# Performance work log

Measured on AMD Instinct MI355X. Metric: run time of the kernel, lower is better.

The kernel has to match this reference:

```python
import jax, jax.numpy as jnp
import numpy as np
from jax import lax

EPS = 1e-5

@jax.custom_vjp
def bin_active(x):
    # forward: sign binarization (original also returns channel-mean of |x|, which is discarded)
    return jnp.sign(x)

def _ba_fwd(x):
    return jnp.sign(x), x

def _ba_bwd(x, g):
    # straight-through estimator: zero grad where |x| >= 1
    return (jnp.where((x >= 1.0) | (x <= -1.0), 0.0, g),)

bin_active.defvjp(_ba_fwd, _ba_bwd)


def setup_inputs() -> dict:
    key = jax.random.key(0)
    k1, k2 = jax.random.split(key)
    N, C_in, H, W_sp = 64, 256, 56, 56
    C_out, K = 256, 3
    x = jax.random.normal(k1, (N, C_in, H, W_sp), dtype=jnp.float32)
    gamma = jnp.ones((C_in,), dtype=jnp.float32)
    beta = jnp.zeros((C_in,), dtype=jnp.float32)
    W = jax.random.normal(k2, (C_out, C_in, K, K), dtype=jnp.float32) * 0.05
    return {"x": x, "gamma": gamma, "beta": beta, "W": W}


def reference(x, gamma, beta, W):
    # BatchNorm2d (training-mode batch stats), affine
    mean = jnp.mean(x, axis=(0, 2, 3), keepdims=True)          # [1,C,1,1]
    var = jnp.var(x, axis=(0, 2, 3), keepdims=True)
    xn = (x - mean) * lax.rsqrt(var + EPS)
    xn = xn * gamma.reshape(1, -1, 1, 1) + beta.reshape(1, -1, 1, 1)
    # binarize activations
    xb = bin_active(xn)
    # Conv2d stride=1 pad=1, no bias, then ReLU
    y = lax.conv_general_dilated(
        xb, W,
        window_strides=(1, 1),
        padding=[(1, 1), (1, 1)],
        dimension_numbers=("NCHW", "OIHW", "NCHW"),
    )
    return jax.nn.relu(y)
```

## Files before the change

kernel.cpp:

```cpp
#include <hip/hip_runtime.h>
#include <hip/hip_bf16.h>
#include <stdint.h>

#define HP 58
#define WP 64
#define CIN 256
#define COUT 256
#define HH 56
#define WW 56
#define IMG_STRIDE (HP*WP*CIN)
#define ROW_STRIDE (WP*CIN)
#define NPIX 200704.0

#define XO    2048
#define XROW  14848
#define AO    93184
#define LDS_TOTAL 158720

typedef __attribute__((ext_vector_type(4))) int i32x4;

#define GLDS(g, l) __builtin_amdgcn_global_load_lds( \
    (const __attribute__((address_space(1))) void*)(g), \
    (__attribute__((address_space(3))) void*)(l), 16, 0, 0)

__global__ __launch_bounds__(256) void stats_partial(const float* __restrict__ x,
                                                     double* __restrict__ part) {
  int b = blockIdx.x;
  int c = b >> 6, n = b & 63;
  const float4* p = (const float4*)(x + (size_t)(n*CIN + c) * (HH*WW));
  double s = 0.0, s2 = 0.0;
  for (int i = threadIdx.x; i < 784; i += 256) {
    float4 v = p[i];
    double a0 = v.x, a1 = v.y, a2 = v.z, a3 = v.w;
    s  += (a0 + a1) + (a2 + a3);
    s2 += (a0*a0 + a1*a1) + (a2*a2 + a3*a3);
  }
  for (int off = 32; off > 0; off >>= 1) {
    s  += __shfl_down(s, off);
    s2 += __shfl_down(s2, off);
  }
  __shared__ double red[8];
  int wv = threadIdx.x >> 6, ln = threadIdx.x & 63;
  if (ln == 0) { red[wv*2] = s; red[wv*2+1] = s2; }
  __syncthreads();
  if (threadIdx.x == 0) {
    double ts = ((red[0]+red[2])+red[4])+red[6];
    double t2 = ((red[1]+red[3])+red[5])+red[7];
    part[(size_t)(c*64 + n)*2]     = ts;
    part[(size_t)(c*64 + n)*2 + 1] = t2;
  }
}

__global__ void stats_final(const double* __restrict__ part,
                            const float* __restrict__ gamma,
                            const float* __restrict__ beta,
                            double* __restrict__ prm) {
  int c = threadIdx.x;
  double s = 0.0, s2 = 0.0;
  for (int n = 0; n < 64; ++n) {
    s  += part[(size_t)(c*64+n)*2];
    s2 += part[(size_t)(c*64+n)*2 + 1];
  }
  double mean = s / NPIX;
  double var  = s2 / NPIX - mean*mean;
  double inv  = 1.0 / sqrt(var + 1e-5);
  prm[c*4+0] = mean;
  prm[c*4+1] = (double)gamma[c] * inv;
  prm[c*4+2] = (double)beta[c];
}

__global__ __launch_bounds__(256) void binarize(const float* __restrict__ x,
                                                const double* __restrict__ prm,
                                                int8_t* __restrict__ xb) {
  int b = blockIdx.x;
  int n = b / HP, y = b % HP;
  int8_t* orow = xb + (size_t)(n*HP + y) * ROW_STRIDE;
  if (y == 0 || y == HP-1) {
    int4 z = {0,0,0,0};
    int4* q = (int4*)orow;
    for (int i = threadIdx.x; i < ROW_STRIDE/16; i += 256) q[i] = z;
    return;
  }
  __shared__ char sbuf[WW][260];
  int h  = y - 1;
  int tid = threadIdx.x;
  #pragma unroll
  for (int it = 0; it < 14; ++it) {
    int t = it*256 + tid;
    int c = t / 14, j = t - c*14;
    float4 v = *(const float4*)(x + (size_t)(n*CIN + c)*(HH*WW) + h*WW + j*4);
    double mu = prm[c*4], gi = prm[c*4+1], be = prm[c*4+2];
    #pragma unroll
    for (int e = 0; e < 4; ++e) {
      double xv = (double)((&v.x)[e]);
      double vv = (xv - mu)*gi + be;
      sbuf[j*4+e][c] = vv > 0.0 ? (int8_t)1 : (vv < 0.0 ? (int8_t)-1 : (int8_t)0);
    }
  }
  __syncthreads();
  int xh = tid >> 6, cq = tid & 63;
  uint32_t* orow32 = (uint32_t*)orow;
  for (int xx0 = 0; xx0 < WP; xx0 += 4) {
    int xx = xx0 + xh;
    uint32_t v = 0;
    if (xx >= 1 && xx <= WW) v = *(const uint32_t*)&sbuf[xx-1][cq*4];
    orow32[xx*64 + cq] = v;
  }
}

__global__ __launch_bounds__(256) void wrepack(const float* __restrict__ W,
                                               int8_t* __restrict__ Wb,
                                               float* __restrict__ invs) {
  int co = blockIdx.x, ci = threadIdx.x;
  float w[9]; float mx = 0.f;
  const float* p = W + (size_t)co*(CIN*9) + ci*9;
  #pragma unroll
  for (int t = 0; t < 9; ++t) { w[t] = p[t]; mx = fmaxf(mx, fabsf(w[t])); }
  for (int off = 32; off > 0; off >>= 1) mx = fmaxf(mx, __shfl_xor(mx, off));
  __shared__ float sm[4];
  if ((threadIdx.x & 63) == 0) sm[threadIdx.x >> 6] = mx;
  __syncthreads();
  mx = fmaxf(fmaxf(sm[0], sm[1]), fmaxf(sm[2], sm[3]));
  float s = mx > 0.f ? 127.f / mx : 0.f;
  #pragma unroll
  for (int t = 0; t < 9; ++t) {
    int q = (int)lrintf(w[t] * s);
    q = q > 127 ? 127 : (q < -127 ? -127 : q);
    Wb[t*(COUT*CIN) + co*CIN + ci] = (int8_t)q;
  }
  if (threadIdx.x == 0) invs[co] = mx / 127.f;
}

__global__ __launch_bounds__(512, 2) void conv_gemm(const int8_t* __restrict__ xb,
                                                    const int8_t* __restrict__ Wb,
                                                    const float* __restrict__ invs,
                                                    float* __restrict__ out) {
  extern __shared__ char smem[];
  int bid = blockIdx.x;
  int swz = (bid & 7) * 112 + (bid >> 3);
  int n_img = swz / 14, rg = swz - n_img * 14;
  int y0 = 1 + rg * 4;

  int tid = threadIdx.x;
  int ln = tid & 63, wid = tid >> 6;
  int wm = wid >> 2, wn = wid & 3;

  size_t xoff = (size_t)n_img * IMG_STRIDE + (size_t)(y0 - 1) * ROW_STRIDE;

  #pragma unroll
  for (int i = 0; i < 11; ++i) {
    int o = tid*16 + i*8192;
    if (o < 89088) {
      int r   = o / XROW;
      int rem = o - r*XROW;
      int xx  = rem >> 8, cb = rem & 255;
      const int8_t* src = xb + xoff + r*ROW_STRIDE + xx*256 + (cb ^ ((xx & 7) << 4));
      GLDS(src, smem + XO + o);
    }
  }

  int arow = tid & 255, aslice = tid >> 8;
  auto STAGE_A = [&](int s, int buf) {
    int sc = s < 36 ? s : 35;
    int tap = sc >> 2, ci0 = (sc & 3) << 6;
    const int8_t* base = Wb + tap*(COUT*CIN) + arow*256 + ci0;
    char* dst = smem + AO + buf*16384 + tid*16;
    GLDS(base + aslice*16,       dst);
    GLDS(base + (2+aslice)*16,   dst + 8192);
  };

  i32x4 acc[8][4] = {};
  STAGE_A(0, 0); STAGE_A(1, 1); STAGE_A(2, 2);

  int afrag = ((ln >> 4) << 12) + (wm*128 + (ln & 15)) * 16;
  int xx0   = ln & 15;
  int cb16  = (ln >> 4) << 4;

  i32x4 aR[2][8], bR[2][4];

  auto LOADF = [&](int s, i32x4 (&av)[8], i32x4 (&bv)[4]) {
    int sc = s < 36 ? s : 35;
    const char* Ab = smem + AO + (s & 3)*16384 + afrag;
    #pragma unroll
    for (int m = 0; m < 8; ++m) av[m] = *(const i32x4*)(Ab + m*256);
    int tap = sc >> 2;
    int kh = (tap * 11) >> 5, kw = tap - kh * 3;
    int cb = ((sc & 3) << 6) + cb16;
    const char* Xr = smem + XO + (wn + kh) * XROW;
    #pragma unroll
    for (int nn = 0; nn < 4; ++nn) {
      int x_in = xx0 + nn*16 + kw - 1;
      bv[nn] = *(const i32x4*)(Xr + x_in*256 + (cb ^ ((x_in & 7) << 4)));
    }
  };

  asm volatile("s_waitcnt vmcnt(4)" ::: "memory");
  __builtin_amdgcn_s_barrier();
  LOADF(0, aR[0], bR[0]);

  auto body = [&](int s, i32x4 (&ac)[8], i32x4 (&bc)[4], i32x4 (&an)[8], i32x4 (&bn)[4]) {
    asm volatile("s_waitcnt vmcnt(2)" ::: "memory");
    __builtin_amdgcn_s_barrier();
    STAGE_A(s + 3, (s + 3) & 3);
    LOADF(s + 1, an, bn);
    __builtin_amdgcn_s_setprio(1);
    #pragma unroll
    for (int m = 0; m < 8; ++m)
      #pragma unroll
      for (int nn = 0; nn < 4; ++nn)
        acc[m][nn] = __builtin_amdgcn_mfma_i32_16x16x64_i8(ac[m], bc[nn], acc[m][nn], 0, 0, 0);
    __builtin_amdgcn_s_setprio(0);
  };

  #pragma unroll 1
  for (int t = 0; t < 18; ++t) {
    body(2*t,     aR[0], bR[0], aR[1], bR[1]);
    body(2*t + 1, aR[1], bR[1], aR[0], bR[0]);
  }

  asm volatile("s_waitcnt vmcnt(0)" ::: "memory");
  __syncthreads();

  float ivv[8][4];
  #pragma unroll
  for (int m = 0; m < 8; ++m)
    #pragma unroll
    for (int r = 0; r < 4; ++r)
      ivv[m][r] = invs[wm*128 + m*16 + (ln >> 4)*4 + r];

  char* eb = smem + wid * 16384;
  int y = y0 + wn;
  size_t obase = (size_t)n_img * COUT * (HH*WW) + (size_t)(y - 1) * WW;

  #pragma unroll
  for (int p = 0; p < 2; ++p) {
    #pragma unroll
    for (int m2 = 0; m2 < 4; ++m2) {
      int m = p*4 + m2;
      #pragma unroll
      for (int nn = 0; nn < 4; ++nn)
        #pragma unroll
        for (int r = 0; r < 4; ++r) {
          int row  = m2*16 + (ln >> 4)*4 + r;
          int slot = (nn*16 + (ln & 15) + 63) & 63;
          int q    = (row >> 2) & 3;
          float v = fmaxf((float)acc[m][nn][r] * ivv[m][r], 0.0f);
          *(float*)(eb + row*256 + (((slot ^ (q << 4))) << 2)) = v;
        }
    }
    int c16 = ln & 15, rq = ln >> 4;
    #pragma unroll
    for (int j = 0; j < 16; ++j) {
      int row = j*4 + rq;
      int q   = (row >> 2) & 3;
      float4 v = *(const float4*)(eb + row*256 + ((c16 << 4) ^ (q << 6)));
      if (c16 < 14) {
        int co = wm*128 + p*64 + row;
        *(float4*)(out + obase + (size_t)co*(HH*WW) + c16*4) = v;
      }
    }
  }
}

extern "C" void kernel_launch(void* const* d_in, const int* in_sizes, int n_in,
                              void* d_out, int out_size, void* d_ws, size_t ws_size,
                              hipStream_t stream) {
  const float* x     = (const float*)d_in[0];
  const float* gamma = (const float*)d_in[1];
  const float* beta  = (const float*)d_in[2];
  const float* W     = (const float*)d_in[3];
  float* out = (float*)d_out;

  char* ws = (char*)d_ws;
  double*  part = (double*)ws;
  double*  prm  = (double*)(ws + 262144);
  float*   invs = (float*)(ws + 270336);
  int8_t*  Wb   = (int8_t*)(ws + 271360);
  int8_t*  xbuf = (int8_t*)(ws + 1048576);

  (void)hipFuncSetAttribute((const void*)conv_gemm,
                            hipFuncAttributeMaxDynamicSharedMemorySize, LDS_TOTAL);

  hipLaunchKernelGGL(wrepack,       dim3(256),    dim3(256), 0, stream, W, Wb, invs);
  hipLaunchKernelGGL(stats_partial, dim3(256*64), dim3(256), 0, stream, x, part);
  hipLaunchKernelGGL(stats_final,   dim3(1),      dim3(256), 0, stream, part, gamma, beta, prm);
  hipLaunchKernelGGL(binarize,      dim3(64*HP),  dim3(256), 0, stream, x, prm, xbuf);
  hipLaunchKernelGGL(conv_gemm,     dim3(896),    dim3(512), LDS_TOTAL, stream, xbuf, Wb, invs, out);
}
```

Measured before the change: 281.9 us.

## Halve conv tile to two output rows with per-wave private weight rings

The implicit-GEMM conv tile shrinks from 4 output rows by 256 channels to 2 rows by 256 channels, which doubles the grid and cuts per-wave accumulators from 8x4 to 4x4 MFMA tiles. Each wave now stages its own 64-channel slice of weights into a private triple-buffered LDS ring, so the per-step block-wide barrier disappears. The goal is to drop barrier stalls and register pressure and to add parallelism. In exchange, weights are reloaded twice as often per output and the input halo overhead per row goes up.

```diff
diff --git a/kernel.cpp b/kernel.cpp
--- a/kernel.cpp
+++ b/kernel.cpp
@@ -12,10 +12,12 @@
 #define ROW_STRIDE (WP*CIN)
 #define NPIX 200704.0
 
-#define XO    2048
+#define XO    256
 #define XROW  14848
-#define AO    93184
-#define LDS_TOTAL 158720
+#define XBYTES (4*XROW)
+#define AO    59648
+#define AWAVE 12288
+#define LDS_TOTAL 157952
 
 typedef __attribute__((ext_vector_type(4))) int i32x4;
 
@@ -137,20 +139,20 @@
                                                     float* __restrict__ out) {
   extern __shared__ char smem[];
   int bid = blockIdx.x;
-  int swz = (bid & 7) * 112 + (bid >> 3);
-  int n_img = swz / 14, rg = swz - n_img * 14;
-  int y0 = 1 + rg * 4;
+  int swz = (bid & 7) * 224 + (bid >> 3);
+  int n_img = swz / 28, rg = swz - n_img * 28;
+  int y0 = 1 + rg * 2;
 
   int tid = threadIdx.x;
   int ln = tid & 63, wid = tid >> 6;
-  int wm = wid >> 2, wn = wid & 3;
+  int wm = wid >> 1, wn = wid & 1;
 
   size_t xoff = (size_t)n_img * IMG_STRIDE + (size_t)(y0 - 1) * ROW_STRIDE;
 
   #pragma unroll
-  for (int i = 0; i < 11; ++i) {
+  for (int i = 0; i < 8; ++i) {
     int o = tid*16 + i*8192;
-    if (o < 89088) {
+    if (o < XBYTES) {
       int r   = o / XROW;
       int rem = o - r*XROW;
       int xx  = rem >> 8, cb = rem & 255;
@@ -159,30 +161,32 @@
     }
   }
 
-  int arow = tid & 255, aslice = tid >> 8;
-  auto STAGE_A = [&](int s, int buf) {
+  char* aring = smem + AO + wid * AWAVE;
+  auto STAGE_A = [&](int s) {
     int sc = s < 36 ? s : 35;
     int tap = sc >> 2, ci0 = (sc & 3) << 6;
-    const int8_t* base = Wb + tap*(COUT*CIN) + arow*256 + ci0;
-    char* dst = smem + AO + buf*16384 + tid*16;
-    GLDS(base + aslice*16,       dst);
-    GLDS(base + (2+aslice)*16,   dst + 8192);
+    const int8_t* src = Wb + tap*(COUT*CIN) + (size_t)(wm*64 + ln)*CIN + ci0;
+    char* dst = aring + (s % 3) * 4096;
+    GLDS(src,      dst);
+    GLDS(src + 16, dst + 1024);
+    GLDS(src + 32, dst + 2048);
+    GLDS(src + 48, dst + 3072);
   };
 
-  i32x4 acc[8][4] = {};
-  STAGE_A(0, 0); STAGE_A(1, 1); STAGE_A(2, 2);
-
-  int afrag = ((ln >> 4) << 12) + (wm*128 + (ln & 15)) * 16;
+  i32x4 acc[4][4] = {};
+  STAGE_A(0); STAGE_A(1); STAGE_A(2);
+  asm volatile("s_waitcnt vmcnt(12)" ::: "memory");
+  __builtin_amdgcn_s_barrier();
+
+  int afrag = ((ln >> 4) << 10) + (ln & 15) * 16;
   int xx0   = ln & 15;
   int cb16  = (ln >> 4) << 4;
 
-  i32x4 aR[2][8], bR[2][4];
-
-  auto LOADF = [&](int s, i32x4 (&av)[8], i32x4 (&bv)[4]) {
+  auto LOADF = [&](int s, i32x4 (&av)[4], i32x4 (&bv)[4]) {
     int sc = s < 36 ? s : 35;
-    const char* Ab = smem + AO + (s & 3)*16384 + afrag;
-    #pragma unroll
-    for (int m = 0; m < 8; ++m) av[m] = *(const i32x4*)(Ab + m*256);
+    const char* Ab = aring + (s % 3) * 4096 + afrag;
+    #pragma unroll
+    for (int m = 0; m < 4; ++m) av[m] = *(const i32x4*)(Ab + m*256);
     int tap = sc >> 2;
     int kh = (tap * 11) >> 5, kw = tap - kh * 3;
     int cb = ((sc & 3) << 6) + cb16;
@@ -194,22 +198,22 @@
     }
   };
 
-  asm volatile("s_waitcnt vmcnt(4)" ::: "memory");
-  __builtin_amdgcn_s_barrier();
+  i32x4 aR[2][4], bR[2][4];
+  asm volatile("s_waitcnt vmcnt(8)" ::: "memory");
   LOADF(0, aR[0], bR[0]);
 
-  auto body = [&](int s, i32x4 (&ac)[8], i32x4 (&bc)[4], i32x4 (&an)[8], i32x4 (&bn)[4]) {
-    asm volatile("s_waitcnt vmcnt(2)" ::: "memory");
-    __builtin_amdgcn_s_barrier();
-    STAGE_A(s + 3, (s + 3) & 3);
-    LOADF(s + 1, an, bn);
+  auto body = [&](int s, i32x4 (&ca)[4], i32x4 (&cb_)[4], i32x4 (&na)[4], i32x4 (&nb)[4]) {
+    asm volatile("s_waitcnt vmcnt(4)" ::: "memory");
+    LOADF(s + 1, na, nb);
     __builtin_amdgcn_s_setprio(1);
     #pragma unroll
-    for (int m = 0; m < 8; ++m)
+    for (int m = 0; m < 4; ++m)
       #pragma unroll
       for (int nn = 0; nn < 4; ++nn)
-        acc[m][nn] = __builtin_amdgcn_mfma_i32_16x16x64_i8(ac[m], bc[nn], acc[m][nn], 0, 0, 0);
+        acc[m][nn] = __builtin_amdgcn_mfma_i32_16x16x64_i8(ca[m], cb_[nn], acc[m][nn], 0, 0, 0);
     __builtin_amdgcn_s_setprio(0);
+    asm volatile("" ::: "memory");
+    STAGE_A(s + 3);
   };
 
   #pragma unroll 1
@@ -218,47 +222,41 @@
     body(2*t + 1, aR[1], bR[1], aR[0], bR[0]);
   }
 
-  asm volatile("s_waitcnt vmcnt(0)" ::: "memory");
-  __syncthreads();
-
-  float ivv[8][4];
-  #pragma unroll
-  for (int m = 0; m < 8; ++m)
+  asm volatile("s_waitcnt vmcnt(0) lgkmcnt(0)" ::: "memory");
+  __builtin_amdgcn_s_barrier();
+
+  float ivv[4][4];
+  #pragma unroll
+  for (int m = 0; m < 4; ++m)
     #pragma unroll
     for (int r = 0; r < 4; ++r)
-      ivv[m][r] = invs[wm*128 + m*16 + (ln >> 4)*4 + r];
+      ivv[m][r] = invs[wm*64 + m*16 + (ln >> 4)*4 + r];
 
   char* eb = smem + wid * 16384;
-  int y = y0 + wn;
-  size_t obase = (size_t)n_img * COUT * (HH*WW) + (size_t)(y - 1) * WW;
-
-  #pragma unroll
-  for (int p = 0; p < 2; ++p) {
-    #pragma unroll
-    for (int m2 = 0; m2 < 4; ++m2) {
-      int m = p*4 + m2;
+  int co0 = wm * 64;
+  size_t obase = (size_t)n_img * COUT * (HH*WW) + (size_t)(y0 + wn - 1) * WW;
+
+  #pragma unroll
+  for (int m = 0; m < 4; ++m)
+    #pragma unroll
+    for (int nn = 0; nn < 4; ++nn)
       #pragma unroll
-      for (int nn = 0; nn < 4; ++nn)
-        #pragma unroll
-        for (int r = 0; r < 4; ++r) {
-          int row  = m2*16 + (ln >> 4)*4 + r;
-          int slot = (nn*16 + (ln & 15) + 63) & 63;
-          int q    = (row >> 2) & 3;
-          float v = fmaxf((float)acc[m][nn][r] * ivv[m][r], 0.0f);
-          *(float*)(eb + row*256 + (((slot ^ (q << 4))) << 2)) = v;
-        }
-    }
-    int c16 = ln & 15, rq = ln >> 4;
-    #pragma unroll
-    for (int j = 0; j < 16; ++j) {
-      int row = j*4 + rq;
-      int q   = (row >> 2) & 3;
-      float4 v = *(const float4*)(eb + row*256 + ((c16 << 4) ^ (q << 6)));
-      if (c16 < 14) {
-        int co = wm*128 + p*64 + row;
-        *(float4*)(out + obase + (size_t)co*(HH*WW) + c16*4) = v;
+      for (int r = 0; r < 4; ++r) {
+        int row  = m*16 + (ln >> 4)*4 + r;
+        int slot = (nn*16 + (ln & 15) + 63) & 63;
+        int q    = (row >> 2) & 3;
+        float v = fmaxf((float)acc[m][nn][r] * ivv[m][r], 0.0f);
+        *(float*)(eb + row*256 + ((slot ^ (q << 4)) << 2)) = v;
       }
-    }
+  asm volatile("s_waitcnt lgkmcnt(0)" ::: "memory");
+  int c16 = ln & 15, rq = ln >> 4;
+  #pragma unroll
+  for (int j = 0; j < 16; ++j) {
+    int row = j*4 + rq;
+    int q   = (row >> 2) & 3;
+    float4 v = *(const float4*)(eb + row*256 + ((c16 << 4) ^ (q << 6)));
+    if (c16 < 14)
+      *(float4*)(out + obase + (size_t)(co0 + row)*(HH*WW) + c16*4) = v;
   }
 }
 
@@ -285,5 +283,5 @@
   hipLaunchKernelGGL(stats_partial, dim3(256*64), dim3(256), 0, stream, x, part);
   hipLaunchKernelGGL(stats_final,   dim3(1),      dim3(256), 0, stream, part, gamma, beta, prm);
   hipLaunchKernelGGL(binarize,      dim3(64*HP),  dim3(256), 0, stream, x, prm, xbuf);
-  hipLaunchKernelGGL(conv_gemm,     dim3(896),    dim3(512), LDS_TOTAL, stream, xbuf, Wb, invs, out);
-}
+  hipLaunchKernelGGL(conv_gemm,     dim3(1792),   dim3(512), LDS_TOTAL, stream, xbuf, Wb, invs, out);
+}
```

Measured after the change: 411.9 us. 46.1% more time.

## Switch conv GEMM to 32x32x32 int8 MFMA with channel-slot activation layout

Applied to the files above, without the earlier changes.

Replaces the 16x16x64 int8 MFMA tiling with 32x32x32 MFMA tiles and repacks both the binarized activations (16-byte channel slots, 58-pixel rows, no padding to 64) and the weights (pre-fragmented per k-slice) so fragments load with plain contiguous reads and no XOR swizzle. The epilogue drops the LDS transpose and writes scaled ReLU outputs straight to global memory. The aim is fewer MFMA issues, cheaper LDS fragment loads and less epilogue staging. In exchange the output stores become scalar and strided across channels, which may coalesce worse, and the new activation layout may cause LDS bank conflicts.

```diff
diff --git a/kernel.cpp b/kernel.cpp
--- a/kernel.cpp
+++ b/kernel.cpp
@@ -3,21 +3,21 @@
 #include <stdint.h>
 
 #define HP 58
-#define WP 64
 #define CIN 256
 #define COUT 256
 #define HH 56
 #define WW 56
-#define IMG_STRIDE (HP*WP*CIN)
-#define ROW_STRIDE (WP*CIN)
+#define XROW 14848
+#define IMG_STRIDE (HP*XROW)
 #define NPIX 200704.0
 
-#define XO    2048
-#define XROW  14848
-#define AO    93184
-#define LDS_TOTAL 158720
-
-typedef __attribute__((ext_vector_type(4))) int i32x4;
+#define XO    16
+#define SROW  928
+#define AO    89600
+#define LDS_TOTAL 155136
+
+typedef __attribute__((ext_vector_type(4)))  int i32x4;
+typedef __attribute__((ext_vector_type(16))) int i32x16;
 
 #define GLDS(g, l) __builtin_amdgcn_global_load_lds( \
     (const __attribute__((address_space(1))) void*)(g), \
@@ -74,11 +74,11 @@
                                                 int8_t* __restrict__ xb) {
   int b = blockIdx.x;
   int n = b / HP, y = b % HP;
-  int8_t* orow = xb + (size_t)(n*HP + y) * ROW_STRIDE;
+  int8_t* orow = xb + (size_t)(n*HP + y) * XROW;
   if (y == 0 || y == HP-1) {
     int4 z = {0,0,0,0};
     int4* q = (int4*)orow;
-    for (int i = threadIdx.x; i < ROW_STRIDE/16; i += 256) q[i] = z;
+    for (int i = threadIdx.x; i < XROW/16; i += 256) q[i] = z;
     return;
   }
   __shared__ char sbuf[WW][260];
@@ -98,18 +98,19 @@
     }
   }
   __syncthreads();
-  int xh = tid >> 6, cq = tid & 63;
-  uint32_t* orow32 = (uint32_t*)orow;
-  for (int xx0 = 0; xx0 < WP; xx0 += 4) {
-    int xx = xx0 + xh;
-    uint32_t v = 0;
-    if (xx >= 1 && xx <= WW) v = *(const uint32_t*)&sbuf[xx-1][cq*4];
-    orow32[xx*64 + cq] = v;
+  for (int u = tid; u < 16*58; u += 256) {
+    int slot = u / 58, xx = u - slot*58;
+    int4 v = {0,0,0,0};
+    if (xx >= 1 && xx <= WW) {
+      const uint32_t* src = (const uint32_t*)&sbuf[xx-1][slot*16];
+      v.x = src[0]; v.y = src[1]; v.z = src[2]; v.w = src[3];
+    }
+    *(int4*)(orow + u*16) = v;
   }
 }
 
 __global__ __launch_bounds__(256) void wrepack(const float* __restrict__ W,
-                                               int8_t* __restrict__ Wb,
+                                               int8_t* __restrict__ Wbr,
                                                float* __restrict__ invs) {
   int co = blockIdx.x, ci = threadIdx.x;
   float w[9]; float mx = 0.f;
@@ -122,17 +123,18 @@
   __syncthreads();
   mx = fmaxf(fmaxf(sm[0], sm[1]), fmaxf(sm[2], sm[3]));
   float s = mx > 0.f ? 127.f / mx : 0.f;
+  int off = ((ci >> 6) * 4 + ((ci >> 4) & 3)) * 4096 + co*16 + (ci & 15);
   #pragma unroll
   for (int t = 0; t < 9; ++t) {
     int q = (int)lrintf(w[t] * s);
     q = q > 127 ? 127 : (q < -127 ? -127 : q);
-    Wb[t*(COUT*CIN) + co*CIN + ci] = (int8_t)q;
+    Wbr[t*65536 + off] = (int8_t)q;
   }
   if (threadIdx.x == 0) invs[co] = mx / 127.f;
 }
 
 __global__ __launch_bounds__(512, 2) void conv_gemm(const int8_t* __restrict__ xb,
-                                                    const int8_t* __restrict__ Wb,
+                                                    const int8_t* __restrict__ Wbr,
                                                     const float* __restrict__ invs,
                                                     float* __restrict__ out) {
   extern __shared__ char smem[];
@@ -145,52 +147,49 @@
   int ln = tid & 63, wid = tid >> 6;
   int wm = wid >> 2, wn = wid & 3;
 
-  size_t xoff = (size_t)n_img * IMG_STRIDE + (size_t)(y0 - 1) * ROW_STRIDE;
+  size_t xoff = (size_t)n_img * IMG_STRIDE + (size_t)(y0 - 1) * XROW;
 
   #pragma unroll
   for (int i = 0; i < 11; ++i) {
     int o = tid*16 + i*8192;
-    if (o < 89088) {
-      int r   = o / XROW;
-      int rem = o - r*XROW;
-      int xx  = rem >> 8, cb = rem & 255;
-      const int8_t* src = xb + xoff + r*ROW_STRIDE + xx*256 + (cb ^ ((xx & 7) << 4));
-      GLDS(src, smem + XO + o);
-    }
-  }
-
-  int arow = tid & 255, aslice = tid >> 8;
+    if (o < 6*XROW)
+      GLDS(xb + xoff + o, smem + XO + o);
+  }
+
   auto STAGE_A = [&](int s, int buf) {
     int sc = s < 36 ? s : 35;
-    int tap = sc >> 2, ci0 = (sc & 3) << 6;
-    const int8_t* base = Wb + tap*(COUT*CIN) + arow*256 + ci0;
+    const int8_t* src = Wbr + (sc >> 2)*65536 + (sc & 3)*16384 + tid*16;
     char* dst = smem + AO + buf*16384 + tid*16;
-    GLDS(base + aslice*16,       dst);
-    GLDS(base + (2+aslice)*16,   dst + 8192);
+    GLDS(src,        dst);
+    GLDS(src + 8192, dst + 8192);
   };
 
-  i32x4 acc[8][4] = {};
+  i32x16 acc[4][2] = {};
   STAGE_A(0, 0); STAGE_A(1, 1); STAGE_A(2, 2);
 
-  int afrag = ((ln >> 4) << 12) + (wm*128 + (ln & 15)) * 16;
-  int xx0   = ln & 15;
-  int cb16  = (ln >> 4) << 4;
-
-  i32x4 aR[2][8], bR[2][4];
-
-  auto LOADF = [&](int s, i32x4 (&av)[8], i32x4 (&bv)[4]) {
+  int afrag = ((ln >> 5) << 12) + (wm*128 + (ln & 31)) * 16;
+  int xx0   = ln & 31;
+  int slotL = ln >> 5;
+
+  i32x4 aR[2][4][2], bR[2][2][2];
+
+  auto LOADF = [&](int s, i32x4 (&av)[4][2], i32x4 (&bv)[2][2]) {
     int sc = s < 36 ? s : 35;
     const char* Ab = smem + AO + (s & 3)*16384 + afrag;
     #pragma unroll
-    for (int m = 0; m < 8; ++m) av[m] = *(const i32x4*)(Ab + m*256);
-    int tap = sc >> 2;
+    for (int mt = 0; mt < 4; ++mt)
+      #pragma unroll
+      for (int ks = 0; ks < 2; ++ks)
+        av[mt][ks] = *(const i32x4*)(Ab + ks*8192 + mt*512);
+    int tap = sc >> 2, q = sc & 3;
     int kh = (tap * 11) >> 5, kw = tap - kh * 3;
-    int cb = ((sc & 3) << 6) + cb16;
     const char* Xr = smem + XO + (wn + kh) * XROW;
     #pragma unroll
-    for (int nn = 0; nn < 4; ++nn) {
-      int x_in = xx0 + nn*16 + kw - 1;
-      bv[nn] = *(const i32x4*)(Xr + x_in*256 + (cb ^ ((x_in & 7) << 4)));
+    for (int nt = 0; nt < 2; ++nt) {
+      int x_in = xx0 + nt*32 + kw - 1;
+      #pragma unroll
+      for (int ks = 0; ks < 2; ++ks)
+        bv[nt][ks] = *(const i32x4*)(Xr + (q*4 + ks*2 + slotL)*SROW + x_in*16);
     }
   };
 
@@ -198,17 +197,21 @@
   __builtin_amdgcn_s_barrier();
   LOADF(0, aR[0], bR[0]);
 
-  auto body = [&](int s, i32x4 (&ac)[8], i32x4 (&bc)[4], i32x4 (&an)[8], i32x4 (&bn)[4]) {
+  auto body = [&](int s, i32x4 (&ca)[4][2], i32x4 (&cb)[2][2],
+                         i32x4 (&na)[4][2], i32x4 (&nb)[2][2]) {
     asm volatile("s_waitcnt vmcnt(2)" ::: "memory");
     __builtin_amdgcn_s_barrier();
     STAGE_A(s + 3, (s + 3) & 3);
-    LOADF(s + 1, an, bn);
+    LOADF(s + 1, na, nb);
     __builtin_amdgcn_s_setprio(1);
     #pragma unroll
-    for (int m = 0; m < 8; ++m)
-      #pragma unroll
-      for (int nn = 0; nn < 4; ++nn)
-        acc[m][nn] = __builtin_amdgcn_mfma_i32_16x16x64_i8(ac[m], bc[nn], acc[m][nn], 0, 0, 0);
+    for (int ks = 0; ks < 2; ++ks)
+      #pragma unroll
+      for (int mt = 0; mt < 4; ++mt)
+        #pragma unroll
+        for (int nt = 0; nt < 2; ++nt)
+          acc[mt][nt] = __builtin_amdgcn_mfma_i32_32x32x32_i8(ca[mt][ks], cb[nt][ks],
+                                                              acc[mt][nt], 0, 0, 0);
     __builtin_amdgcn_s_setprio(0);
   };
 
@@ -217,46 +220,27 @@
     body(2*t,     aR[0], bR[0], aR[1], bR[1]);
     body(2*t + 1, aR[1], bR[1], aR[0], bR[0]);
   }
-
   asm volatile("s_waitcnt vmcnt(0)" ::: "memory");
-  __syncthreads();
-
-  float ivv[8][4];
-  #pragma unroll
-  for (int m = 0; m < 8; ++m)
-    #pragma unroll
-    for (int r = 0; r < 4; ++r)
-      ivv[m][r] = invs[wm*128 + m*16 + (ln >> 4)*4 + r];
-
-  char* eb = smem + wid * 16384;
-  int y = y0 + wn;
-  size_t obase = (size_t)n_img * COUT * (HH*WW) + (size_t)(y - 1) * WW;
-
-  #pragma unroll
-  for (int p = 0; p < 2; ++p) {
-    #pragma unroll
-    for (int m2 = 0; m2 < 4; ++m2) {
-      int m = p*4 + m2;
-      #pragma unroll
-      for (int nn = 0; nn < 4; ++nn)
-        #pragma unroll
-        for (int r = 0; r < 4; ++r) {
-          int row  = m2*16 + (ln >> 4)*4 + r;
-          int slot = (nn*16 + (ln & 15) + 63) & 63;
-          int q    = (row >> 2) & 3;
-          float v = fmaxf((float)acc[m][nn][r] * ivv[m][r], 0.0f);
-          *(float*)(eb + row*256 + (((slot ^ (q << 4))) << 2)) = v;
-        }
-    }
-    int c16 = ln & 15, rq = ln >> 4;
-    #pragma unroll
-    for (int j = 0; j < 16; ++j) {
-      int row = j*4 + rq;
-      int q   = (row >> 2) & 3;
-      float4 v = *(const float4*)(eb + row*256 + ((c16 << 4) ^ (q << 6)));
-      if (c16 < 14) {
-        int co = wm*128 + p*64 + row;
-        *(float4*)(out + obase + (size_t)co*(HH*WW) + c16*4) = v;
+
+  int y_out = y0 + wn - 1;
+  size_t ob0 = ((size_t)n_img * COUT) * (HH*WW) + (size_t)y_out * WW;
+  #pragma unroll
+  for (int mt = 0; mt < 4; ++mt) {
+    int cb0 = wm*128 + mt*32 + ((ln >> 5) << 2);
+    float4 iv[4];
+    #pragma unroll
+    for (int q = 0; q < 4; ++q) iv[q] = *(const float4*)(invs + cb0 + 8*q);
+    #pragma unroll
+    for (int nt = 0; nt < 2; ++nt) {
+      int xx = nt*32 + (ln & 31);
+      bool ok = (xx >= 1) && (xx <= WW);
+      size_t ob = ob0 + (xx - 1);
+      #pragma unroll
+      for (int r = 0; r < 16; ++r) {
+        int q = r >> 2, rr = r & 3;
+        int co = cb0 + 8*q + rr;
+        float v = fmaxf((float)acc[mt][nt][r] * ((&iv[q].x)[rr]), 0.0f);
+        if (ok) out[ob + (size_t)co * (HH*WW)] = v;
       }
     }
   }
@@ -275,15 +259,15 @@
   double*  part = (double*)ws;
   double*  prm  = (double*)(ws + 262144);
   float*   invs = (float*)(ws + 270336);
-  int8_t*  Wb   = (int8_t*)(ws + 271360);
+  int8_t*  Wbr  = (int8_t*)(ws + 271360);
   int8_t*  xbuf = (int8_t*)(ws + 1048576);
 
   (void)hipFuncSetAttribute((const void*)conv_gemm,
                             hipFuncAttributeMaxDynamicSharedMemorySize, LDS_TOTAL);
 
-  hipLaunchKernelGGL(wrepack,       dim3(256),    dim3(256), 0, stream, W, Wb, invs);
+  hipLaunchKernelGGL(wrepack,       dim3(256),    dim3(256), 0, stream, W, Wbr, invs);
   hipLaunchKernelGGL(stats_partial, dim3(256*64), dim3(256), 0, stream, x, part);
   hipLaunchKernelGGL(stats_final,   dim3(1),      dim3(256), 0, stream, part, gamma, beta, prm);
   hipLaunchKernelGGL(binarize,      dim3(64*HP),  dim3(256), 0, stream, x, prm, xbuf);
-  hipLaunchKernelGGL(conv_gemm,     dim3(896),    dim3(512), LDS_TOTAL, stream, xbuf, Wb, invs, out);
-}
+  hipLaunchKernelGGL(conv_gemm,     dim3(896),    dim3(512), LDS_TOTAL, stream, xbuf, Wbr, invs, out);
+}
```

New measurement: 283.2 us. About the same (+0.5%).
